# Kernel tuning notes

Measured on AMD Instinct MI355X. Metric: run time of the kernel, lower is better.

The kernel has to match this reference:

```python
import jax, jax.numpy as jnp
import numpy as np

N, E, HN, K = 4096, 8192, 1024, 8
NF, EF = 128, 64
NH = [256, 256]
EH = [64, 64]
EMB = NH[-1] + len(EH)  # 258
BN_EPS = 1e-5


def setup_inputs() -> dict:
    key = jax.random.key(0)
    ks = jax.random.split(key, 16)

    def nrm(k, shape, fan):
        return jax.random.normal(k, shape, jnp.float32) / np.float32(np.sqrt(fan))

    return {
        "X_n": jax.random.normal(ks[0], (N, NF), jnp.float32),
        "X_e": jax.random.normal(ks[1], (E, EF), jnp.float32),
        # row-normalized-ish adjacency and scaled Laplacian to keep activations bounded
        "A_tilde": jax.random.uniform(ks[2], (N, N), jnp.float32) / np.float32(N),
        "L1_tilde": jax.random.normal(ks[3], (E, E), jnp.float32) / np.float32(np.sqrt(E)),
        "B1": jax.random.normal(ks[4], (N, E), jnp.float32) / np.float32(np.sqrt(E)),
        # GNN params (Linear stores weight as [out, in])
        "gnn_W1": nrm(ks[5], (NH[0], NF), NF), "gnn_b1": jnp.zeros((NH[0],), jnp.float32),
        "gnn_W2": nrm(ks[6], (NH[1], NH[0]), NH[0]), "gnn_b2": jnp.zeros((NH[1],), jnp.float32),
        # HoSC layer 1: in=EF, out=EH[0]
        "hosc_W1": nrm(ks[7], (EH[0], EF), EF), "hosc_b1": jnp.zeros((EH[0],), jnp.float32),
        "bn1_g": jnp.ones((EH[0],), jnp.float32), "bn1_b": jnp.zeros((EH[0],), jnp.float32),
        # HoSC layer 2: in=1 (after channel-max), out=EH[1]
        "hosc_W2": nrm(ks[8], (EH[1], 1), 1), "hosc_b2": jnp.zeros((EH[1],), jnp.float32),
        "bn2_g": jnp.ones((EH[1],), jnp.float32), "bn2_b": jnp.zeros((EH[1],), jnp.float32),
        # heads
        "node_W": nrm(ks[9], (1, EMB), EMB), "node_b": jnp.zeros((1,), jnp.float32),
        "edge_W": nrm(ks[10], (1, len(EH)), len(EH)), "edge_b": jnp.zeros((1,), jnp.float32),
        "hyper_W": nrm(ks[11], (1, EMB), EMB), "hyper_b": jnp.zeros((1,), jnp.float32),
        "hyperedges": jax.random.randint(ks[12], (HN, K), 0, N, jnp.int64),
    }


def _bn(x, g, b):
    # training-mode BatchNorm1d: biased batch statistics over rows
    m = jnp.mean(x, axis=0)
    v = jnp.var(x, axis=0)
    return g * (x - m) / jnp.sqrt(v + BN_EPS) + b


def _hosc_layer(Z, L1, W, bias, g, b):
    Zt = Z @ W.T + bias            # [E, out]
    Zc = L1 @ Zt                   # [E, out]
    Zp = jax.nn.relu(_bn(Zc, g, b))
    return jnp.max(Zp, axis=1, keepdims=True)  # [E, 1]


def reference(X_n, X_e, A_tilde, L1_tilde, B1,
              gnn_W1, gnn_b1, gnn_W2, gnn_b2,
              hosc_W1, hosc_b1, bn1_g, bn1_b,
              hosc_W2, hosc_b2, bn2_g, bn2_b,
              node_W, node_b, edge_W, edge_b, hyper_W, hyper_b,
              hyperedges):
    # --- GNN over nodes ---
    H = jax.nn.relu((A_tilde @ X_n) @ gnn_W1.T + gnn_b1)   # [N, 256]
    H_n = jax.nn.relu((A_tilde @ H) @ gnn_W2.T + gnn_b2)   # [N, 256]

    # --- HoSC over edges ---
    Z1 = _hosc_layer(X_e, L1_tilde, hosc_W1, hosc_b1, bn1_g, bn1_b)  # [E, 1]
    Z2 = _hosc_layer(Z1, L1_tilde, hosc_W2, hosc_b2, bn2_g, bn2_b)   # [E, 1]
    Z_H = jnp.concatenate([Z1, Z2], axis=1)                 # [E, 2]

    # --- fuse edge info into nodes ---
    H_e = B1 @ Z_H                                          # [N, 2]
    Hcat = jnp.concatenate([H_n, H_e], axis=1)              # [N, 258]

    node_prob = jax.nn.sigmoid(Hcat @ node_W.T + node_b).squeeze(-1)  # [N]
    edge_prob = jax.nn.sigmoid(Z_H @ edge_W.T + edge_b).squeeze(-1)   # [E]

    # vectorized hyperedge gather-mean-linear-sigmoid (fixed-size hyperedges)
    hfeat = Hcat[hyperedges].mean(axis=1)                   # [HN, 258]
    hyperedge_prob = jax.nn.sigmoid(hfeat @ hyper_W.T + hyper_b)  # [HN, 1]

    return node_prob, edge_prob, hyperedge_prob, Hcat
```

## Files before the change

kernel.cpp:

```cpp
#include <hip/hip_runtime.h>
#include <hip/hip_bf16.h>

using f32x4  = __attribute__((ext_vector_type(4))) float;
using u32x4  = __attribute__((ext_vector_type(4))) unsigned int;
using bf16x8 = __attribute__((ext_vector_type(8))) short;

__device__ __forceinline__ ushort f2bf(float x) {
    union { __hip_bfloat16 h; ushort u; } cv;
    cv.h = __float2bfloat16(x);
    return cv.u;
}
__device__ __forceinline__ unsigned pk2(float lo, float hi) {
    return (unsigned)f2bf(lo) | ((unsigned)f2bf(hi) << 16);
}
__device__ __forceinline__ float sigmoidf_(float x) { return 1.f / (1.f + expf(-x)); }

template<bool A_BF16, bool SPLIT, bool RELU, bool BF16_OUT, bool HAS_BIAS>
__global__ __launch_bounds__(256)
void gemm_kernel(const void* __restrict__ Avoid, const ushort* __restrict__ B,
                 const float* __restrict__ bias, float* __restrict__ Cf,
                 ushort* __restrict__ Cb, int M, int N, int K, int ldc, int kPerChunk)
{
    __shared__ ushort As[128 * 40];
    __shared__ ushort Bs[64 * 40];
    const int tid  = threadIdx.x;
    const int lane = tid & 63;
    const int wid  = tid >> 6;
    const int wr   = wid >> 1, wc = wid & 1;
    const int g    = lane >> 4, lr = lane & 15;
    const long m0  = (long)blockIdx.x * 128;
    const int  n0  = blockIdx.y * 64;

    int kbeg = 0, kend = K;
    if (SPLIT) { kbeg = blockIdx.z * kPerChunk; kend = kbeg + kPerChunk; if (kend > K) kend = K; }

    const int bkr = tid & 31;
    const int bcb = tid >> 5;

    const float*  Af = (const float*)Avoid;
    const ushort* Ab = (const ushort*)Avoid;

    f32x4 pa[4];
    u32x4 pab[2];
    u32x4 pb;

    auto loadT = [&](int k0) {
        if (A_BF16) {
#pragma unroll
            for (int i = 0; i < 2; i++) {
                int s = tid + 256 * i; int row = s >> 2, c8 = s & 3;
                pab[i] = *(const u32x4*)(Ab + (m0 + row) * (long)K + k0 + c8 * 8);
            }
        } else {
#pragma unroll
            for (int i = 0; i < 4; i++) {
                int s = tid + 256 * i; int row = s >> 3, c4 = s & 7;
                pa[i] = *(const f32x4*)(Af + (m0 + row) * (long)K + k0 + c4 * 4);
            }
        }
        pb = *(const u32x4*)(B + (long)(k0 + bkr) * N + n0 + bcb * 8);
    };
    auto storeT = [&]() {
        if (A_BF16) {
#pragma unroll
            for (int i = 0; i < 2; i++) {
                int s = tid + 256 * i; int row = s >> 2, c8 = s & 3;
                *(u32x4*)(&As[row * 40 + c8 * 8]) = pab[i];
            }
        } else {
#pragma unroll
            for (int i = 0; i < 4; i++) {
                int s = tid + 256 * i; int row = s >> 3, c4 = s & 7;
                ushort4 w;
                w.x = f2bf(pa[i].x); w.y = f2bf(pa[i].y);
                w.z = f2bf(pa[i].z); w.w = f2bf(pa[i].w);
                *(ushort4*)(&As[row * 40 + c4 * 4]) = w;
            }
        }
        const ushort* p8 = (const ushort*)&pb;
#pragma unroll
        for (int j = 0; j < 8; j++) Bs[(bcb * 8 + j) * 40 + bkr] = p8[j];
    };

    f32x4 acc[4][2] = {};

    const int nk = (kend - kbeg) >> 5;
    loadT(kbeg);
    for (int t = 0; t < nk; ++t) {
        storeT();
        __syncthreads();
        if (t + 1 < nk) loadT(kbeg + ((t + 1) << 5));
        bf16x8 af[4], bfr[2];
#pragma unroll
        for (int fm = 0; fm < 4; fm++)
            af[fm] = *(const bf16x8*)(&As[(wr * 64 + fm * 16 + lr) * 40 + g * 8]);
#pragma unroll
        for (int fn = 0; fn < 2; fn++)
            bfr[fn] = *(const bf16x8*)(&Bs[(wc * 32 + fn * 16 + lr) * 40 + g * 8]);
#pragma unroll
        for (int fm = 0; fm < 4; fm++)
#pragma unroll
            for (int fn = 0; fn < 2; fn++)
                acc[fm][fn] = __builtin_amdgcn_mfma_f32_16x16x32_bf16(af[fm], bfr[fn], acc[fm][fn], 0, 0, 0);
        __syncthreads();
    }

    if (SPLIT) {
        float* P = Cf + (long)blockIdx.z * M * N;
#pragma unroll
        for (int fm = 0; fm < 4; fm++)
#pragma unroll
            for (int fn = 0; fn < 2; fn++)
#pragma unroll
                for (int rr = 0; rr < 4; rr++) {
                    long row = m0 + wr * 64 + fm * 16 + g * 4 + rr;
                    int  col = n0 + wc * 32 + fn * 16 + lr;
                    P[row * N + col] = acc[fm][fn][rr];
                }
    } else {
#pragma unroll
        for (int fm = 0; fm < 4; fm++)
#pragma unroll
            for (int fn = 0; fn < 2; fn++)
#pragma unroll
                for (int rr = 0; rr < 4; rr++) {
                    long row = m0 + wr * 64 + fm * 16 + g * 4 + rr;
                    int  col = n0 + wc * 32 + fn * 16 + lr;
                    float v = acc[fm][fn][rr];
                    if (HAS_BIAS) v += bias[col];
                    if (RELU) v = fmaxf(v, 0.f);
                    if (BF16_OUT) Cb[row * ldc + col] = f2bf(v);
                    else          Cf[row * ldc + col] = v;
                }
    }
}

__global__ __launch_bounds__(256) void reduce_add_bf16(const float* __restrict__ P,
                                                       ushort* __restrict__ C, int MN, int nz)
{
    int i = blockIdx.x * 256 + threadIdx.x;
    int n4 = MN >> 2;
    if (i >= n4) return;
    f32x4 a = ((const f32x4*)P)[i];
    for (int z = 1; z < nz; z++) a += ((const f32x4*)(P + (long)z * MN))[i];
    ushort4 o; o.x = f2bf(a.x); o.y = f2bf(a.y); o.z = f2bf(a.z); o.w = f2bf(a.w);
    ((ushort4*)C)[i] = o;
}

__global__ __launch_bounds__(256) void prep_k(const float* __restrict__ A, ushort* __restrict__ Abf,
                                              const float* __restrict__ Xn, ushort* __restrict__ Xnb,
                                              const float* __restrict__ W1, ushort* __restrict__ W1t,
                                              const float* __restrict__ W2, ushort* __restrict__ W2t,
                                              const float* __restrict__ Wh, ushort* __restrict__ Wht,
                                              float* __restrict__ stats)
{
    int b = blockIdx.x, t = threadIdx.x;
    if (b < 8192) {
        long j = (long)b * 256 + t;
        f32x4 v0 = ((const f32x4*)A)[2 * j];
        f32x4 v1 = ((const f32x4*)A)[2 * j + 1];
        u32x4 w;
        w.x = pk2(v0.x, v0.y); w.y = pk2(v0.z, v0.w);
        w.z = pk2(v1.x, v1.y); w.w = pk2(v1.z, v1.w);
        ((u32x4*)Abf)[j] = w;
    } else if (b < 8448) {
        long j = (long)(b - 8192) * 256 + t;
        f32x4 v0 = ((const f32x4*)Xn)[2 * j];
        f32x4 v1 = ((const f32x4*)Xn)[2 * j + 1];
        u32x4 w;
        w.x = pk2(v0.x, v0.y); w.y = pk2(v0.z, v0.w);
        w.z = pk2(v1.x, v1.y); w.w = pk2(v1.z, v1.w);
        ((u32x4*)Xnb)[j] = w;
    } else if (b < 8576) {
        int j = (b - 8448) * 256 + t;
        int i = j >> 8, o = j & 255;
        W1t[j] = f2bf(W1[o * 128 + i]);
    } else if (b < 8832) {
        int j = (b - 8576) * 256 + t;
        int i = j >> 8, o = j & 255;
        W2t[j] = f2bf(W2[o * 256 + i]);
    } else if (b < 8848) {
        int j = (b - 8832) * 256 + t;
        int i = j >> 6, o = j & 63;
        Wht[j] = f2bf(Wh[o * 64 + i]);
    } else {
        if (t < 192) stats[t] = 0.f;
    }
}

__global__ __launch_bounds__(256) void bnred_k(const float* __restrict__ P,
                                               float* __restrict__ Zc,
                                               float* __restrict__ gsum, float* __restrict__ gsq)
{
    const int MN = 8192 * 64;
    int b = blockIdx.x, t = threadIdx.x;
    int c = t & 63, rg = t >> 6;
    float sx = 0.f, sq = 0.f;
    int base = b * 32 + rg;
#pragma unroll 4
    for (int i = 0; i < 8; i++) {
        long idx = (long)(base + 4 * i) * 64 + c;
        float x = P[idx] + P[idx + MN] + P[idx + 2 * MN] + P[idx + 3 * MN];
        Zc[idx] = x;
        sx += x; sq += x * x;
    }
    __shared__ float ls[256], lq[256];
    ls[t] = sx; lq[t] = sq;
    __syncthreads();
    if (t < 64) {
        float a = ls[t] + ls[t + 64] + ls[t + 128] + ls[t + 192];
        float q = lq[t] + lq[t + 64] + lq[t + 128] + lq[t + 192];
        atomicAdd(&gsum[t], a);
        atomicAdd(&gsq[t], q);
    }
}

__global__ __launch_bounds__(256) void z1_k(const float* __restrict__ Zc,
                                            const float* __restrict__ gsum, const float* __restrict__ gsq,
                                            const float* __restrict__ g, const float* __restrict__ b,
                                            float* __restrict__ Z1)
{
    int w = threadIdx.x >> 6, lane = threadIdx.x & 63;
    int row = blockIdx.x * 4 + w;
    const float inv = 1.f / 8192.f;
    float m = gsum[lane] * inv;
    float v = gsq[lane] * inv - m * m;
    float x = Zc[row * 64 + lane];
    float y = fmaxf(g[lane] * (x - m) * rsqrtf(v + 1e-5f) + b[lane], 0.f);
#pragma unroll
    for (int o = 32; o > 0; o >>= 1) y = fmaxf(y, __shfl_xor(y, o));
    if (lane == 0) Z1[row] = y;
}

__global__ __launch_bounds__(256) void pass2_k(const float* __restrict__ L1, const float* __restrict__ Z1,
                                               float* __restrict__ s, float* __restrict__ r)
{
    int row = blockIdx.x, t = threadIdx.x;
    int l = t & 63, w = t >> 6;
    const f32x4* rp = (const f32x4*)(L1 + (long)row * 8192);
    const f32x4* z4 = (const f32x4*)Z1;
    float as = 0.f, ar = 0.f;
#pragma unroll 4
    for (int k = 0; k < 8; k++) {
        f32x4 v = rp[t + 256 * k];
        f32x4 z = z4[t + 256 * k];
        as += v.x * z.x + v.y * z.y + v.z * z.z + v.w * z.w;
        ar += v.x + v.y + v.z + v.w;
    }
#pragma unroll
    for (int o = 32; o > 0; o >>= 1) { as += __shfl_xor(as, o); ar += __shfl_xor(ar, o); }
    __shared__ float sw[4], rw[4];
    if (l == 0) { sw[w] = as; rw[w] = ar; }
    __syncthreads();
    if (t == 0) {
        s[row] = sw[0] + sw[1] + sw[2] + sw[3];
        r[row] = rw[0] + rw[1] + rw[2] + rw[3];
    }
}

__global__ __launch_bounds__(256) void stats2_k(const float* __restrict__ s, const float* __restrict__ r,
                                                float* __restrict__ S5)
{
    int t = threadIdx.x, l = t & 63, w = t >> 6;
    float Ss = 0, Sr = 0, Sss = 0, Srr = 0, Ssr = 0;
    for (int i = t; i < 8192; i += 256) {
        float sv = s[i], rv = r[i];
        Ss += sv; Sr += rv; Sss += sv * sv; Srr += rv * rv; Ssr += sv * rv;
    }
#pragma unroll
    for (int o = 32; o > 0; o >>= 1) {
        Ss += __shfl_xor(Ss, o); Sr += __shfl_xor(Sr, o);
        Sss += __shfl_xor(Sss, o); Srr += __shfl_xor(Srr, o); Ssr += __shfl_xor(Ssr, o);
    }
    __shared__ float buf[4][5];
    if (l == 0) { buf[w][0] = Ss; buf[w][1] = Sr; buf[w][2] = Sss; buf[w][3] = Srr; buf[w][4] = Ssr; }
    __syncthreads();
    if (t < 5) S5[t] = buf[0][t] + buf[1][t] + buf[2][t] + buf[3][t];
}

__global__ __launch_bounds__(256) void z2_edge_k(const float* __restrict__ s, const float* __restrict__ r,
                                                 const float* __restrict__ S,
                                                 const float* __restrict__ W2, const float* __restrict__ b2,
                                                 const float* __restrict__ g2, const float* __restrict__ bb2,
                                                 const float* __restrict__ eW, const float* __restrict__ eb,
                                                 const float* __restrict__ Z1,
                                                 float* __restrict__ Z2, float* __restrict__ edge_out)
{
    int w = threadIdx.x >> 6, lane = threadIdx.x & 63;
    int row = blockIdx.x * 4 + w;
    const float inv = 1.f / 8192.f;
    float ms = S[0] * inv, mr = S[1] * inv;
    float vs = S[2] * inv - ms * ms;
    float vr = S[3] * inv - mr * mr;
    float cv = S[4] * inv - ms * mr;
    float w2 = W2[lane], bz = b2[lane];
    float mc = w2 * ms + bz * mr;
    float vc = w2 * w2 * vs + 2.f * w2 * bz * cv + bz * bz * vr;
    float x  = w2 * s[row] + bz * r[row];
    float y  = fmaxf(g2[lane] * (x - mc) * rsqrtf(vc + 1e-5f) + bb2[lane], 0.f);
#pragma unroll
    for (int o = 32; o > 0; o >>= 1) y = fmaxf(y, __shfl_xor(y, o));
    if (lane == 0) {
        Z2[row] = y;
        float e = Z1[row] * eW[0] + y * eW[1] + eb[0];
        edge_out[row] = sigmoidf_(e);
    }
}

__global__ __launch_bounds__(256) void he_node_k(const float* __restrict__ B1, const float* __restrict__ Z1,
                                                 const float* __restrict__ Z2, float* __restrict__ hcat,
                                                 const float* __restrict__ nW, const float* __restrict__ nb,
                                                 float* __restrict__ node_out)
{
    int n = blockIdx.x, t = threadIdx.x;
    int l = t & 63, w = t >> 6;
    const f32x4* rp  = (const f32x4*)(B1 + (long)n * 8192);
    const f32x4* z1v = (const f32x4*)Z1;
    const f32x4* z2v = (const f32x4*)Z2;
    float a1 = 0.f, a2 = 0.f;
#pragma unroll 4
    for (int k = 0; k < 8; k++) {
        f32x4 v = rp[t + 256 * k];
        f32x4 p = z1v[t + 256 * k];
        f32x4 q = z2v[t + 256 * k];
        a1 += v.x * p.x + v.y * p.y + v.z * p.z + v.w * p.w;
        a2 += v.x * q.x + v.y * q.y + v.z * q.z + v.w * q.w;
    }
    float d = hcat[(long)n * 258 + t] * nW[t];
#pragma unroll
    for (int o = 32; o > 0; o >>= 1) {
        a1 += __shfl_xor(a1, o); a2 += __shfl_xor(a2, o); d += __shfl_xor(d, o);
    }
    __shared__ float s1[4], s2[4], s3[4];
    if (l == 0) { s1[w] = a1; s2[w] = a2; s3[w] = d; }
    __syncthreads();
    if (t == 0) {
        float A1 = s1[0] + s1[1] + s1[2] + s1[3];
        float A2 = s2[0] + s2[1] + s2[2] + s2[3];
        float D  = s3[0] + s3[1] + s3[2] + s3[3];
        hcat[(long)n * 258 + 256] = A1;
        hcat[(long)n * 258 + 257] = A2;
        node_out[n] = sigmoidf_(D + A1 * nW[256] + A2 * nW[257] + nb[0]);
    }
}

__global__ __launch_bounds__(256) void hyper_k(const void* __restrict__ he_idx,
                                               const float* __restrict__ hcat,
                                               const float* __restrict__ hW, const float* __restrict__ hb,
                                               float* __restrict__ out)
{
    int w = threadIdx.x >> 6, lane = threadIdx.x & 63;
    int h = blockIdx.x * 4 + w;
    const unsigned int* u = (const unsigned int*)he_idx;
    unsigned int odd = u[2 * lane + 1];
    bool is64 = __all(odd == 0u);
    float acc = 0.f;
    for (int k = 0; k < 8; k++) {
        int idx;
        if (is64) idx = (int)((const long long*)he_idx)[h * 8 + k];
        else      idx = ((const int*)he_idx)[h * 8 + k];
        const float* hr = hcat + (long)idx * 258;
        for (int d = lane; d < 258; d += 64) acc += hr[d] * hW[d];
    }
    acc *= 0.125f;
#pragma unroll
    for (int o = 32; o > 0; o >>= 1) acc += __shfl_xor(acc, o);
    if (lane == 0) out[h] = sigmoidf_(acc + hb[0]);
}

extern "C" void kernel_launch(void* const* d_in, const int* in_sizes, int n_in,
                              void* d_out, int out_size, void* d_ws, size_t ws_size,
                              hipStream_t stream)
{
    const float* X_n  = (const float*)d_in[0];
    const float* X_e  = (const float*)d_in[1];
    const float* A_t  = (const float*)d_in[2];
    const float* L1   = (const float*)d_in[3];
    const float* B1   = (const float*)d_in[4];
    const float* gW1  = (const float*)d_in[5];
    const float* gb1  = (const float*)d_in[6];
    const float* gW2  = (const float*)d_in[7];
    const float* gb2  = (const float*)d_in[8];
    const float* hW1  = (const float*)d_in[9];
    const float* hb1  = (const float*)d_in[10];
    const float* bn1g = (const float*)d_in[11];
    const float* bn1b = (const float*)d_in[12];
    const float* hW2  = (const float*)d_in[13];
    const float* hb2  = (const float*)d_in[14];
    const float* bn2g = (const float*)d_in[15];
    const float* bn2b = (const float*)d_in[16];
    const float* nW   = (const float*)d_in[17];
    const float* nb   = (const float*)d_in[18];
    const float* eW   = (const float*)d_in[19];
    const float* ebb  = (const float*)d_in[20];
    const float* yW   = (const float*)d_in[21];
    const float* yb   = (const float*)d_in[22];
    const void*  he   = d_in[23];

    float* out       = (float*)d_out;
    float* out_node  = out;
    float* out_edge  = out + 4096;
    float* out_hyper = out + 12288;
    float* hcat      = out + 13312;

    size_t off = 0;
    auto alloc = [&](size_t bytes) {
        void* p = (char*)d_ws + off;
        off = (off + bytes + 255) & ~(size_t)255;
        return p;
    };
    ushort* Abf   = (ushort*)alloc((size_t)4096 * 4096 * 2);
    ushort* Xn_bf = (ushort*)alloc(4096 * 128 * 2);
    ushort* W1t   = (ushort*)alloc(128 * 256 * 2);
    ushort* W2t   = (ushort*)alloc(256 * 256 * 2);
    ushort* W1ht  = (ushort*)alloc(64 * 64 * 2);
    ushort* C1b   = (ushort*)alloc(4096 * 128 * 2);
    ushort* H_bf  = (ushort*)alloc(4096 * 256 * 2);
    ushort* C2b   = (ushort*)alloc(4096 * 256 * 2);
    ushort* Zt1   = (ushort*)alloc(8192 * 64 * 2);
    float*  Zc1   = (float*)alloc(8192 * 64 * 4);
    float*  stats = (float*)alloc(256 * 4);
    float*  gsum  = stats;
    float*  gsq   = stats + 64;
    float*  S5    = stats + 128;
    float*  Z1    = (float*)alloc(8192 * 4);
    float*  Z2    = (float*)alloc(8192 * 4);
    float*  sbuf  = (float*)alloc(8192 * 4);
    float*  rbuf  = (float*)alloc(8192 * 4);
    float*  P     = (float*)alloc((size_t)2097152 * 4);

    prep_k<<<8849, 256, 0, stream>>>(A_t, Abf, X_n, Xn_bf, gW1, W1t, gW2, W2t, hW1, W1ht, stats);

    gemm_kernel<true, true, false, false, false><<<dim3(32, 2, 4), 256, 0, stream>>>(
        Abf, Xn_bf, nullptr, P, nullptr, 4096, 128, 4096, 128, 1024);
    reduce_add_bf16<<<512, 256, 0, stream>>>(P, C1b, 4096 * 128, 4);
    gemm_kernel<true, false, true, true, true><<<dim3(32, 4, 1), 256, 0, stream>>>(
        C1b, W1t, gb1, nullptr, H_bf, 4096, 256, 128, 256, 0);
    gemm_kernel<true, true, false, false, false><<<dim3(32, 4, 2), 256, 0, stream>>>(
        Abf, H_bf, nullptr, P, nullptr, 4096, 256, 4096, 256, 2048);
    reduce_add_bf16<<<1024, 256, 0, stream>>>(P, C2b, 4096 * 256, 2);
    gemm_kernel<true, false, true, false, true><<<dim3(32, 4, 1), 256, 0, stream>>>(
        C2b, W2t, gb2, hcat, nullptr, 4096, 256, 256, 258, 0);

    gemm_kernel<false, false, false, true, true><<<dim3(64, 1, 1), 256, 0, stream>>>(
        X_e, W1ht, hb1, nullptr, Zt1, 8192, 64, 64, 64, 0);
    gemm_kernel<false, true, false, false, false><<<dim3(64, 1, 4), 256, 0, stream>>>(
        L1, Zt1, nullptr, P, nullptr, 8192, 64, 8192, 64, 2048);
    bnred_k<<<256, 256, 0, stream>>>(P, Zc1, gsum, gsq);
    z1_k<<<2048, 256, 0, stream>>>(Zc1, gsum, gsq, bn1g, bn1b, Z1);

    pass2_k<<<8192, 256, 0, stream>>>(L1, Z1, sbuf, rbuf);
    stats2_k<<<1, 256, 0, stream>>>(sbuf, rbuf, S5);
    z2_edge_k<<<2048, 256, 0, stream>>>(sbuf, rbuf, S5, hW2, hb2, bn2g, bn2b,
                                        eW, ebb, Z1, Z2, out_edge);

    he_node_k<<<4096, 256, 0, stream>>>(B1, Z1, Z2, hcat, nW, nb, out_node);
    hyper_k<<<256, 256, 0, stream>>>(he, hcat, yW, yb, out_hyper);
}
```

Before: 293.9 us.

## Pre-convert L1 to bf16 and reuse it for the HoSC GEMM and pass2

Adds a bf16 conversion of the 8192x8192 L1 matrix to the prep kernel. Both the layer-1 HoSC GEMM (now on the bf16 A path, split-K 8) and the pass2 row-dot kernel then read the half-size copy. This aims to speed up the GEMM's A loads and halve pass2 traffic. In exchange it adds a full fp32 read plus bf16 write of L1, a larger partial buffer, and bf16 rounding error in the second HoSC layer.

```diff
diff --git a/kernel.cpp b/kernel.cpp
--- a/kernel.cpp
+++ b/kernel.cpp
@@ -12,6 +12,12 @@
 }
 __device__ __forceinline__ unsigned pk2(float lo, float hi) {
     return (unsigned)f2bf(lo) | ((unsigned)f2bf(hi) << 16);
+}
+__device__ __forceinline__ float bflo(unsigned u) {
+    union { unsigned i; float f; } c; c.i = u << 16; return c.f;
+}
+__device__ __forceinline__ float bfhi(unsigned u) {
+    union { unsigned i; float f; } c; c.i = u & 0xFFFF0000u; return c.f;
 }
 __device__ __forceinline__ float sigmoidf_(float x) { return 1.f / (1.f + expf(-x)); }
 
@@ -147,7 +153,8 @@
     ((ushort4*)C)[i] = o;
 }
 
-__global__ __launch_bounds__(256) void prep_k(const float* __restrict__ A, ushort* __restrict__ Abf,
+__global__ __launch_bounds__(256) void prep_k(const float* __restrict__ L1, ushort* __restrict__ L1b,
+                                              const float* __restrict__ A, ushort* __restrict__ Abf,
                                               const float* __restrict__ Xn, ushort* __restrict__ Xnb,
                                               const float* __restrict__ W1, ushort* __restrict__ W1t,
                                               const float* __restrict__ W2, ushort* __restrict__ W2t,
@@ -155,32 +162,40 @@
                                               float* __restrict__ stats)
 {
     int b = blockIdx.x, t = threadIdx.x;
-    if (b < 8192) {
+    if (b < 32768) {
         long j = (long)b * 256 + t;
+        f32x4 v0 = ((const f32x4*)L1)[2 * j];
+        f32x4 v1 = ((const f32x4*)L1)[2 * j + 1];
+        u32x4 w;
+        w.x = pk2(v0.x, v0.y); w.y = pk2(v0.z, v0.w);
+        w.z = pk2(v1.x, v1.y); w.w = pk2(v1.z, v1.w);
+        ((u32x4*)L1b)[j] = w;
+    } else if (b < 40960) {
+        long j = (long)(b - 32768) * 256 + t;
         f32x4 v0 = ((const f32x4*)A)[2 * j];
         f32x4 v1 = ((const f32x4*)A)[2 * j + 1];
         u32x4 w;
         w.x = pk2(v0.x, v0.y); w.y = pk2(v0.z, v0.w);
         w.z = pk2(v1.x, v1.y); w.w = pk2(v1.z, v1.w);
         ((u32x4*)Abf)[j] = w;
-    } else if (b < 8448) {
-        long j = (long)(b - 8192) * 256 + t;
+    } else if (b < 41216) {
+        long j = (long)(b - 40960) * 256 + t;
         f32x4 v0 = ((const f32x4*)Xn)[2 * j];
         f32x4 v1 = ((const f32x4*)Xn)[2 * j + 1];
         u32x4 w;
         w.x = pk2(v0.x, v0.y); w.y = pk2(v0.z, v0.w);
         w.z = pk2(v1.x, v1.y); w.w = pk2(v1.z, v1.w);
         ((u32x4*)Xnb)[j] = w;
-    } else if (b < 8576) {
-        int j = (b - 8448) * 256 + t;
+    } else if (b < 41344) {
+        int j = (b - 41216) * 256 + t;
         int i = j >> 8, o = j & 255;
         W1t[j] = f2bf(W1[o * 128 + i]);
-    } else if (b < 8832) {
-        int j = (b - 8576) * 256 + t;
+    } else if (b < 41600) {
+        int j = (b - 41344) * 256 + t;
         int i = j >> 8, o = j & 255;
         W2t[j] = f2bf(W2[o * 256 + i]);
-    } else if (b < 8848) {
-        int j = (b - 8832) * 256 + t;
+    } else if (b < 41616) {
+        int j = (b - 41600) * 256 + t;
         int i = j >> 6, o = j & 63;
         Wht[j] = f2bf(Wh[o * 64 + i]);
     } else {
@@ -192,7 +207,7 @@
                                                float* __restrict__ Zc,
                                                float* __restrict__ gsum, float* __restrict__ gsq)
 {
-    const int MN = 8192 * 64;
+    const long MN = 8192 * 64;
     int b = blockIdx.x, t = threadIdx.x;
     int c = t & 63, rg = t >> 6;
     float sx = 0.f, sq = 0.f;
@@ -200,7 +215,9 @@
 #pragma unroll 4
     for (int i = 0; i < 8; i++) {
         long idx = (long)(base + 4 * i) * 64 + c;
-        float x = P[idx] + P[idx + MN] + P[idx + 2 * MN] + P[idx + 3 * MN];
+        float x = 0.f;
+#pragma unroll
+        for (int z = 0; z < 8; z++) x += P[idx + z * MN];
         Zc[idx] = x;
         sx += x; sq += x * x;
     }
@@ -232,20 +249,26 @@
     if (lane == 0) Z1[row] = y;
 }
 
-__global__ __launch_bounds__(256) void pass2_k(const float* __restrict__ L1, const float* __restrict__ Z1,
+__global__ __launch_bounds__(256) void pass2_k(const ushort* __restrict__ L1b, const float* __restrict__ Z1,
                                                float* __restrict__ s, float* __restrict__ r)
 {
     int row = blockIdx.x, t = threadIdx.x;
     int l = t & 63, w = t >> 6;
-    const f32x4* rp = (const f32x4*)(L1 + (long)row * 8192);
+    const u32x4* rp = (const u32x4*)(L1b + (long)row * 8192);
     const f32x4* z4 = (const f32x4*)Z1;
     float as = 0.f, ar = 0.f;
-#pragma unroll 4
-    for (int k = 0; k < 8; k++) {
-        f32x4 v = rp[t + 256 * k];
-        f32x4 z = z4[t + 256 * k];
-        as += v.x * z.x + v.y * z.y + v.z * z.z + v.w * z.w;
-        ar += v.x + v.y + v.z + v.w;
+#pragma unroll 2
+    for (int k = 0; k < 4; k++) {
+        int j = t + 256 * k;
+        u32x4 v = rp[j];
+        f32x4 za = z4[2 * j], zb = z4[2 * j + 1];
+        float x0 = bflo(v.x), x1 = bfhi(v.x);
+        float x2 = bflo(v.y), x3 = bfhi(v.y);
+        float x4 = bflo(v.z), x5 = bfhi(v.z);
+        float x6 = bflo(v.w), x7 = bfhi(v.w);
+        as += x0 * za.x + x1 * za.y + x2 * za.z + x3 * za.w
+            + x4 * zb.x + x5 * zb.y + x6 * zb.z + x7 * zb.w;
+        ar += x0 + x1 + x2 + x3 + x4 + x5 + x6 + x7;
     }
 #pragma unroll
     for (int o = 32; o > 0; o >>= 1) { as += __shfl_xor(as, o); ar += __shfl_xor(ar, o); }
@@ -409,6 +432,7 @@
         off = (off + bytes + 255) & ~(size_t)255;
         return p;
     };
+    ushort* L1bf  = (ushort*)alloc((size_t)8192 * 8192 * 2);
     ushort* Abf   = (ushort*)alloc((size_t)4096 * 4096 * 2);
     ushort* Xn_bf = (ushort*)alloc(4096 * 128 * 2);
     ushort* W1t   = (ushort*)alloc(128 * 256 * 2);
@@ -427,9 +451,10 @@
     float*  Z2    = (float*)alloc(8192 * 4);
     float*  sbuf  = (float*)alloc(8192 * 4);
     float*  rbuf  = (float*)alloc(8192 * 4);
-    float*  P     = (float*)alloc((size_t)2097152 * 4);
-
-    prep_k<<<8849, 256, 0, stream>>>(A_t, Abf, X_n, Xn_bf, gW1, W1t, gW2, W2t, hW1, W1ht, stats);
+    float*  P     = (float*)alloc((size_t)8192 * 64 * 8 * 4);
+
+    prep_k<<<41617, 256, 0, stream>>>(L1, L1bf, A_t, Abf, X_n, Xn_bf,
+                                      gW1, W1t, gW2, W2t, hW1, W1ht, stats);
 
     gemm_kernel<true, true, false, false, false><<<dim3(32, 2, 4), 256, 0, stream>>>(
         Abf, Xn_bf, nullptr, P, nullptr, 4096, 128, 4096, 128, 1024);
@@ -444,12 +469,12 @@
 
     gemm_kernel<false, false, false, true, true><<<dim3(64, 1, 1), 256, 0, stream>>>(
         X_e, W1ht, hb1, nullptr, Zt1, 8192, 64, 64, 64, 0);
-    gemm_kernel<false, true, false, false, false><<<dim3(64, 1, 4), 256, 0, stream>>>(
-        L1, Zt1, nullptr, P, nullptr, 8192, 64, 8192, 64, 2048);
+    gemm_kernel<true, true, false, false, false><<<dim3(64, 1, 8), 256, 0, stream>>>(
+        L1bf, Zt1, nullptr, P, nullptr, 8192, 64, 8192, 64, 1024);
     bnred_k<<<256, 256, 0, stream>>>(P, Zc1, gsum, gsq);
     z1_k<<<2048, 256, 0, stream>>>(Zc1, gsum, gsq, bn1g, bn1b, Z1);
 
-    pass2_k<<<8192, 256, 0, stream>>>(L1, Z1, sbuf, rbuf);
+    pass2_k<<<8192, 256, 0, stream>>>(L1bf, Z1, sbuf, rbuf);
     stats2_k<<<1, 256, 0, stream>>>(sbuf, rbuf, S5);
     z2_edge_k<<<2048, 256, 0, stream>>>(sbuf, rbuf, S5, hW2, hb2, bn2g, bn2b,
                                         eW, ebb, Z1, Z2, out_edge);
```

Measured after the change: 297.1 us. About the same (+1.1%).

## Fuse split-K reductions into consumer GEMMs and fold small kernels into prep

Applied to the files above, without the earlier changes.

The separate split-K reduce kernels are removed. The following small GEMMs now sum the fp32 partial buffers while loading their A tiles. The X_e·W1 linear layer moves into prep_k as a scalar dot product, stats2_k is replaced by atomics inside pass2_k, and the L1 GEMM split-K is raised from 4 to 8. This cuts kernel launches and intermediate bf16 round-trips. In exchange it adds more partial-buffer traffic and more atomics, and changes rounding because the intermediates are now fp32 rather than bf16.

```diff
diff --git a/kernel.cpp b/kernel.cpp
--- a/kernel.cpp
+++ b/kernel.cpp
@@ -15,11 +15,12 @@
 }
 __device__ __forceinline__ float sigmoidf_(float x) { return 1.f / (1.f + expf(-x)); }
 
-template<bool A_BF16, bool SPLIT, bool RELU, bool BF16_OUT, bool HAS_BIAS>
+template<int NSUM, bool A_BF16, bool SPLIT, bool RELU, bool BF16_OUT, bool HAS_BIAS>
 __global__ __launch_bounds__(256)
 void gemm_kernel(const void* __restrict__ Avoid, const ushort* __restrict__ B,
                  const float* __restrict__ bias, float* __restrict__ Cf,
-                 ushort* __restrict__ Cb, int M, int N, int K, int ldc, int kPerChunk)
+                 ushort* __restrict__ Cb, int M, int N, int K, int ldc,
+                 int kPerChunk, long pStride)
 {
     __shared__ ushort As[128 * 40];
     __shared__ ushort Bs[64 * 40];
@@ -55,7 +56,13 @@
 #pragma unroll
             for (int i = 0; i < 4; i++) {
                 int s = tid + 256 * i; int row = s >> 3, c4 = s & 7;
-                pa[i] = *(const f32x4*)(Af + (m0 + row) * (long)K + k0 + c4 * 4);
+                const float* base = Af + (m0 + row) * (long)K + k0 + c4 * 4;
+                f32x4 v = *(const f32x4*)base;
+                if (NSUM > 0) {
+#pragma unroll
+                    for (int z = 1; z < NSUM; z++) v += *(const f32x4*)(base + z * pStride);
+                }
+                pa[i] = v;
             }
         }
         pb = *(const u32x4*)(B + (long)(k0 + bkr) * N + n0 + bcb * 8);
@@ -135,23 +142,12 @@
     }
 }
 
-__global__ __launch_bounds__(256) void reduce_add_bf16(const float* __restrict__ P,
-                                                       ushort* __restrict__ C, int MN, int nz)
-{
-    int i = blockIdx.x * 256 + threadIdx.x;
-    int n4 = MN >> 2;
-    if (i >= n4) return;
-    f32x4 a = ((const f32x4*)P)[i];
-    for (int z = 1; z < nz; z++) a += ((const f32x4*)(P + (long)z * MN))[i];
-    ushort4 o; o.x = f2bf(a.x); o.y = f2bf(a.y); o.z = f2bf(a.z); o.w = f2bf(a.w);
-    ((ushort4*)C)[i] = o;
-}
-
 __global__ __launch_bounds__(256) void prep_k(const float* __restrict__ A, ushort* __restrict__ Abf,
                                               const float* __restrict__ Xn, ushort* __restrict__ Xnb,
                                               const float* __restrict__ W1, ushort* __restrict__ W1t,
                                               const float* __restrict__ W2, ushort* __restrict__ W2t,
-                                              const float* __restrict__ Wh, ushort* __restrict__ Wht,
+                                              const float* __restrict__ Xe, const float* __restrict__ Wh,
+                                              const float* __restrict__ hb, ushort* __restrict__ Zt1,
                                               float* __restrict__ stats)
 {
     int b = blockIdx.x, t = threadIdx.x;
@@ -179,10 +175,15 @@
         int j = (b - 8576) * 256 + t;
         int i = j >> 8, o = j & 255;
         W2t[j] = f2bf(W2[o * 256 + i]);
-    } else if (b < 8848) {
-        int j = (b - 8832) * 256 + t;
-        int i = j >> 6, o = j & 63;
-        Wht[j] = f2bf(Wh[o * 64 + i]);
+    } else if (b < 10880) {
+        int row = (b - 8832) * 4 + (t >> 6);
+        int o   = t & 63;
+        const float* xr = Xe + (long)row * 64;
+        const float* wr = Wh + (long)o * 64;
+        float acc = hb[o];
+#pragma unroll 8
+        for (int i = 0; i < 64; i++) acc += xr[i] * wr[i];
+        Zt1[(long)row * 64 + o] = f2bf(acc);
     } else {
         if (t < 192) stats[t] = 0.f;
     }
@@ -192,7 +193,7 @@
                                                float* __restrict__ Zc,
                                                float* __restrict__ gsum, float* __restrict__ gsq)
 {
-    const int MN = 8192 * 64;
+    const long MN = 8192 * 64;
     int b = blockIdx.x, t = threadIdx.x;
     int c = t & 63, rg = t >> 6;
     float sx = 0.f, sq = 0.f;
@@ -200,7 +201,9 @@
 #pragma unroll 4
     for (int i = 0; i < 8; i++) {
         long idx = (long)(base + 4 * i) * 64 + c;
-        float x = P[idx] + P[idx + MN] + P[idx + 2 * MN] + P[idx + 3 * MN];
+        float x = 0.f;
+#pragma unroll
+        for (int z = 0; z < 8; z++) x += P[idx + z * MN];
         Zc[idx] = x;
         sx += x; sq += x * x;
     }
@@ -233,7 +236,8 @@
 }
 
 __global__ __launch_bounds__(256) void pass2_k(const float* __restrict__ L1, const float* __restrict__ Z1,
-                                               float* __restrict__ s, float* __restrict__ r)
+                                               float* __restrict__ s, float* __restrict__ r,
+                                               float* __restrict__ S5)
 {
     int row = blockIdx.x, t = threadIdx.x;
     int l = t & 63, w = t >> 6;
@@ -253,29 +257,13 @@
     if (l == 0) { sw[w] = as; rw[w] = ar; }
     __syncthreads();
     if (t == 0) {
-        s[row] = sw[0] + sw[1] + sw[2] + sw[3];
-        r[row] = rw[0] + rw[1] + rw[2] + rw[3];
-    }
-}
-
-__global__ __launch_bounds__(256) void stats2_k(const float* __restrict__ s, const float* __restrict__ r,
-                                                float* __restrict__ S5)
-{
-    int t = threadIdx.x, l = t & 63, w = t >> 6;
-    float Ss = 0, Sr = 0, Sss = 0, Srr = 0, Ssr = 0;
-    for (int i = t; i < 8192; i += 256) {
-        float sv = s[i], rv = r[i];
-        Ss += sv; Sr += rv; Sss += sv * sv; Srr += rv * rv; Ssr += sv * rv;
-    }
-#pragma unroll
-    for (int o = 32; o > 0; o >>= 1) {
-        Ss += __shfl_xor(Ss, o); Sr += __shfl_xor(Sr, o);
-        Sss += __shfl_xor(Sss, o); Srr += __shfl_xor(Srr, o); Ssr += __shfl_xor(Ssr, o);
-    }
-    __shared__ float buf[4][5];
-    if (l == 0) { buf[w][0] = Ss; buf[w][1] = Sr; buf[w][2] = Sss; buf[w][3] = Srr; buf[w][4] = Ssr; }
-    __syncthreads();
-    if (t < 5) S5[t] = buf[0][t] + buf[1][t] + buf[2][t] + buf[3][t];
+        float S = sw[0] + sw[1] + sw[2] + sw[3];
+        float R = rw[0] + rw[1] + rw[2] + rw[3];
+        s[row] = S; r[row] = R;
+        atomicAdd(&S5[0], S);     atomicAdd(&S5[1], R);
+        atomicAdd(&S5[2], S * S); atomicAdd(&S5[3], R * R);
+        atomicAdd(&S5[4], S * R);
+    }
 }
 
 __global__ __launch_bounds__(256) void z2_edge_k(const float* __restrict__ s, const float* __restrict__ r,
@@ -413,10 +401,6 @@
     ushort* Xn_bf = (ushort*)alloc(4096 * 128 * 2);
     ushort* W1t   = (ushort*)alloc(128 * 256 * 2);
     ushort* W2t   = (ushort*)alloc(256 * 256 * 2);
-    ushort* W1ht  = (ushort*)alloc(64 * 64 * 2);
-    ushort* C1b   = (ushort*)alloc(4096 * 128 * 2);
-    ushort* H_bf  = (ushort*)alloc(4096 * 256 * 2);
-    ushort* C2b   = (ushort*)alloc(4096 * 256 * 2);
     ushort* Zt1   = (ushort*)alloc(8192 * 64 * 2);
     float*  Zc1   = (float*)alloc(8192 * 64 * 4);
     float*  stats = (float*)alloc(256 * 4);
@@ -427,33 +411,29 @@
     float*  Z2    = (float*)alloc(8192 * 4);
     float*  sbuf  = (float*)alloc(8192 * 4);
     float*  rbuf  = (float*)alloc(8192 * 4);
-    float*  P     = (float*)alloc((size_t)2097152 * 4);
-
-    prep_k<<<8849, 256, 0, stream>>>(A_t, Abf, X_n, Xn_bf, gW1, W1t, gW2, W2t, hW1, W1ht, stats);
-
-    gemm_kernel<true, true, false, false, false><<<dim3(32, 2, 4), 256, 0, stream>>>(
-        Abf, Xn_bf, nullptr, P, nullptr, 4096, 128, 4096, 128, 1024);
-    reduce_add_bf16<<<512, 256, 0, stream>>>(P, C1b, 4096 * 128, 4);
-    gemm_kernel<true, false, true, true, true><<<dim3(32, 4, 1), 256, 0, stream>>>(
-        C1b, W1t, gb1, nullptr, H_bf, 4096, 256, 128, 256, 0);
-    gemm_kernel<true, true, false, false, false><<<dim3(32, 4, 2), 256, 0, stream>>>(
-        Abf, H_bf, nullptr, P, nullptr, 4096, 256, 4096, 256, 2048);
-    reduce_add_bf16<<<1024, 256, 0, stream>>>(P, C2b, 4096 * 256, 2);
-    gemm_kernel<true, false, true, false, true><<<dim3(32, 4, 1), 256, 0, stream>>>(
-        C2b, W2t, gb2, hcat, nullptr, 4096, 256, 256, 258, 0);
-
-    gemm_kernel<false, false, false, true, true><<<dim3(64, 1, 1), 256, 0, stream>>>(
-        X_e, W1ht, hb1, nullptr, Zt1, 8192, 64, 64, 64, 0);
-    gemm_kernel<false, true, false, false, false><<<dim3(64, 1, 4), 256, 0, stream>>>(
-        L1, Zt1, nullptr, P, nullptr, 8192, 64, 8192, 64, 2048);
+    float*  P     = (float*)alloc((size_t)8192 * 64 * 8 * 4);
+
+    prep_k<<<10881, 256, 0, stream>>>(A_t, Abf, X_n, Xn_bf, gW1, W1t, gW2, W2t,
+                                      X_e, hW1, hb1, Zt1, stats);
+
+    gemm_kernel<0, true, true, false, false, false><<<dim3(32, 2, 4), 256, 0, stream>>>(
+        Abf, Xn_bf, nullptr, P, nullptr, 4096, 128, 4096, 128, 1024, 0);
+    gemm_kernel<4, false, false, true, true, true><<<dim3(32, 4, 1), 256, 0, stream>>>(
+        P, W1t, gb1, nullptr, (ushort*)Zc1 , 4096, 256, 128, 256, 0,
+        (long)4096 * 128);
+    ushort* H_bf = (ushort*)Zc1;
+    gemm_kernel<0, true, true, false, false, false><<<dim3(32, 4, 2), 256, 0, stream>>>(
+        Abf, H_bf, nullptr, P, nullptr, 4096, 256, 4096, 256, 2048, 0);
+    gemm_kernel<2, false, false, true, false, true><<<dim3(32, 4, 1), 256, 0, stream>>>(
+        P, W2t, gb2, hcat, nullptr, 4096, 256, 256, 258, 0, (long)4096 * 256);
+
+    gemm_kernel<0, false, true, false, false, false><<<dim3(64, 1, 8), 256, 0, stream>>>(
+        L1, Zt1, nullptr, P, nullptr, 8192, 64, 8192, 64, 1024, 0);
     bnred_k<<<256, 256, 0, stream>>>(P, Zc1, gsum, gsq);
     z1_k<<<2048, 256, 0, stream>>>(Zc1, gsum, gsq, bn1g, bn1b, Z1);
-
-    pass2_k<<<8192, 256, 0, stream>>>(L1, Z1, sbuf, rbuf);
-    stats2_k<<<1, 256, 0, stream>>>(sbuf, rbuf, S5);
+    pass2_k<<<8192, 256, 0, stream>>>(L1, Z1, sbuf, rbuf, S5);
     z2_edge_k<<<2048, 256, 0, stream>>>(sbuf, rbuf, S5, hW2, hb2, bn2g, bn2b,
                                         eW, ebb, Z1, Z2, out_edge);
-
     he_node_k<<<4096, 256, 0, stream>>>(B1, Z1, Z2, hcat, nW, nb, out_node);
     hyper_k<<<256, 256, 0, stream>>>(he, hcat, yW, yb, out_hyper);
 }
```

New measurement: 785.5 us. 2.67x slower.
